# Kernel optimization log

Measured on AMD Instinct MI355X. Metric: run time of the kernel, lower is better.

Reference implementation:

```python
import jax, jax.numpy as jnp
import numpy as np

B, N, C, H = 4, 2048, 768, 12
D = C // H  # head_dim = 64

def setup_inputs() -> dict:
    key = jax.random.key(0)
    ks = jax.random.split(key, 6)
    s = 0.02
    return {
        "img_tokens": jax.random.normal(ks[0], (B, N, C), jnp.float32),
        "ln_gamma": jnp.ones((C,), jnp.float32),
        "ln_beta": jnp.zeros((C,), jnp.float32),
        "w_qkv": jax.random.normal(ks[1], (C, 3 * C), jnp.float32) * s,
        "w_out": jax.random.normal(ks[2], (C, C), jnp.float32) * s,
        "b_out": jnp.zeros((C,), jnp.float32),
    }

def reference(img_tokens, ln_gamma, ln_beta, w_qkv, w_out, b_out):
    x = img_tokens
    # LayerNorm over channel dim
    mu = jnp.mean(x, axis=-1, keepdims=True)
    var = jnp.var(x, axis=-1, keepdims=True)
    xn = (x - mu) * jax.lax.rsqrt(var + 1e-5) * ln_gamma + ln_beta
    qkv = xn @ w_qkv                      # [B, N, 3C]
    q, k, v = jnp.split(qkv, 3, axis=-1)
    def heads(t):                          # [B, N, C] -> [B, H, N, D]
        return t.reshape(B, N, H, D).transpose(0, 2, 1, 3)
    q, k, v = heads(q), heads(k), heads(v)
    scale = 1.0 / np.sqrt(D).astype(np.float32)
    scores = jnp.einsum('bhnd,bhmd->bhnm', q, k) * scale  # [B, H, N, N]
    attn = jax.nn.softmax(scores, axis=-1)
    out = jnp.einsum('bhnm,bhmd->bhnd', attn, v)          # [B, H, N, D]
    out = out.transpose(0, 2, 1, 3).reshape(B, N, C)
    out = out @ w_out + b_out
    return out + img_tokens
```

## Files before the change

kernel.cpp:

```cpp
#include <hip/hip_runtime.h>


typedef __bf16 bf16x8 __attribute__((ext_vector_type(8)));
typedef float  f32x4  __attribute__((ext_vector_type(4)));

#define MFMA16(a,b,c) __builtin_amdgcn_mfma_f32_16x16x32_bf16((a),(b),(c),0,0,0)

__device__ inline f32x4 zero4() { f32x4 z = {0.f,0.f,0.f,0.f}; return z; }

__device__ inline void gll16(const __bf16* g, __bf16* l) {
  __builtin_amdgcn_global_load_lds((const __attribute__((address_space(1))) unsigned int*)g,
                                   (__attribute__((address_space(3))) unsigned int*)l,
                                   16, 0, 0);
}

__device__ inline __bf16 bf16_trunc(float f) {
  const unsigned int u = __builtin_bit_cast(unsigned int, f);
  return __builtin_bit_cast(__bf16, (unsigned short)(u >> 16));
}

__global__ __launch_bounds__(256) void ln_kernel(const float* __restrict__ x,
                                                 const float* __restrict__ g,
                                                 const float* __restrict__ bt,
                                                 __bf16* __restrict__ xn) {
  const int row = blockIdx.x;
  const int tid = threadIdx.x;
  const float* xr = x + (size_t)row * 768;
  float v[3]; float s = 0.f, ss = 0.f;
  #pragma unroll
  for (int i = 0; i < 3; ++i) { float f = xr[tid + 256*i]; v[i] = f; s += f; ss += f*f; }
  #pragma unroll
  for (int m = 32; m >= 1; m >>= 1) { s += __shfl_xor(s, m, 64); ss += __shfl_xor(ss, m, 64); }
  __shared__ float red[8];
  const int wave = tid >> 6;
  if ((tid & 63) == 0) { red[wave] = s; red[4 + wave] = ss; }
  __syncthreads();
  s  = red[0] + red[1] + red[2] + red[3];
  ss = red[4] + red[5] + red[6] + red[7];
  const float mu  = s * (1.f/768.f);
  const float var = ss * (1.f/768.f) - mu*mu;
  const float inv = rsqrtf(var + 1e-5f);
  __bf16* xo = xn + (size_t)row * 768;
  #pragma unroll
  for (int i = 0; i < 3; ++i) {
    const int c0 = tid + 256*i;
    xo[c0] = (__bf16)((v[i] - mu) * inv * g[c0] + bt[c0]);
  }
}

__global__ __launch_bounds__(256) void transpose_kernel(const float* __restrict__ in,
                                                        __bf16* __restrict__ out,
                                                        int R, int C) {
  __shared__ float t[32][33];
  const int tx = threadIdx.x & 31, ty = threadIdx.x >> 5;
  const int c0 = blockIdx.x * 32, r0 = blockIdx.y * 32;
  #pragma unroll
  for (int p = 0; p < 4; ++p) t[ty + 8*p][tx] = in[(size_t)(r0 + ty + 8*p) * C + c0 + tx];
  __syncthreads();
  #pragma unroll
  for (int p = 0; p < 4; ++p) out[(size_t)(c0 + ty + 8*p) * R + r0 + tx] = (__bf16)t[tx][ty + 8*p];
}

template<int KDIM>
__device__ inline void gemm_mainloop(const __bf16* __restrict__ A, const __bf16* __restrict__ BT,
                                     int bm, int bn, int wave, int lane,
                                     f32x4 acc[4][4], __bf16* Asm, __bf16* Bsm) {
  const int wm = wave >> 1, wn = wave & 1;
  const int lr = lane & 15, lk = lane >> 4;
  for (int k0 = 0; k0 < KDIM; k0 += 32) {
    #pragma unroll
    for (int s2 = 0; s2 < 2; ++s2) {
      const int blk = wave * 2 + s2;
      gll16(A  + (size_t)(bm + blk*16 + lr) * KDIM + k0 + lk*8, Asm + blk*512);
      gll16(BT + (size_t)(bn + blk*16 + lr) * KDIM + k0 + lk*8, Bsm + blk*512);
    }
    __builtin_amdgcn_s_waitcnt(0);
    __syncthreads();
    bf16x8 a[4], b[4];
    #pragma unroll
    for (int mt = 0; mt < 4; ++mt) a[mt] = *(const bf16x8*)(Asm + (wm*4+mt)*512 + lane*8);
    #pragma unroll
    for (int nt = 0; nt < 4; ++nt) b[nt] = *(const bf16x8*)(Bsm + (wn*4+nt)*512 + lane*8);
    #pragma unroll
    for (int mt = 0; mt < 4; ++mt)
      #pragma unroll
      for (int nt = 0; nt < 4; ++nt)
        acc[mt][nt] = MFMA16(a[mt], b[nt], acc[mt][nt]);
    __syncthreads();
  }
}

__global__ __launch_bounds__(256) void gemm_qkv_kernel(const __bf16* __restrict__ A,
                                                       const __bf16* __restrict__ BT,
                                                       __bf16* __restrict__ q,
                                                       __bf16* __restrict__ k,
                                                       __bf16* __restrict__ vt) {
  __shared__ __align__(16) __bf16 smem[128*66 + 256];
  __bf16* Asm = smem;
  __bf16* Bsm = smem + 4096;
  const int lane = threadIdx.x & 63, wave = threadIdx.x >> 6;
  const int bm = blockIdx.y * 128, bn = blockIdx.x * 128;
  f32x4 acc[4][4];
  #pragma unroll
  for (int i = 0; i < 4; ++i)
    #pragma unroll
    for (int j = 0; j < 4; ++j) acc[i][j] = zero4();
  gemm_mainloop<768>(A, BT, bm, bn, wave, lane, acc, Asm, Bsm);
  const int wm = wave >> 1, wn = wave & 1;
  const int quad = lane >> 4, c = lane & 15;
  if (bn < 1536) {
    const float qscale = 0.125f * 1.44269504088896f;
    #pragma unroll
    for (int mt = 0; mt < 4; ++mt)
      #pragma unroll
      for (int nt = 0; nt < 4; ++nt) {
        const int col = bn + wn*64 + nt*16 + c;
        const int which = col >> 9 >= 1 && col >= 768 ? 1 : 0;
        const int within = col - which*768;
        const int h = within >> 6, d = within & 63;
        #pragma unroll
        for (int r = 0; r < 4; ++r) {
          const int row = bm + wm*64 + mt*16 + quad*4 + r;
          const int b = row >> 11, n = row & 2047;
          const float vv = acc[mt][nt][r];
          const size_t idx = ((size_t)(b*12 + h) * 2048 + n) * 64 + d;
          if (which == 0) q[idx] = (__bf16)(vv * qscale);
          else            k[idx] = (__bf16)vv;
        }
      }
  } else {
    #pragma unroll
    for (int mt = 0; mt < 4; ++mt)
      #pragma unroll
      for (int nt = 0; nt < 4; ++nt) {
        const int lcol = wn*64 + nt*16 + c;
        #pragma unroll
        for (int r = 0; r < 4; ++r) {
          const int lrow = wm*64 + mt*16 + quad*4 + r;
          smem[lrow*66 + lcol] = (__bf16)acc[mt][nt][r];
        }
      }
    __syncthreads();
    const int b = bm >> 11, n0 = bm & 2047;
    const int vo = bn - 1536;
    const int n = threadIdx.x & 127;
    const int csel = threadIdx.x >> 7;
    #pragma unroll
    for (int pass = 0; pass < 64; ++pass) {
      const int lc = pass*2 + csel;
      const int gcol = vo + lc;
      const int h = gcol >> 6, d = gcol & 63;
      vt[((size_t)(b*12 + h)*64 + d)*2048 + n0 + n] = smem[n*66 + lc];
    }
  }
}

__global__ __launch_bounds__(256) void gemm_out_kernel(const __bf16* __restrict__ A,
                                                       const __bf16* __restrict__ BT,
                                                       const float* __restrict__ bias,
                                                       const float* __restrict__ resid,
                                                       float* __restrict__ out) {
  __shared__ __align__(16) __bf16 Asm[8*512];
  __shared__ __align__(16) __bf16 Bsm[8*512];
  const int lane = threadIdx.x & 63, wave = threadIdx.x >> 6;
  const int bm = blockIdx.y * 128, bn = blockIdx.x * 128;
  f32x4 acc[4][4];
  #pragma unroll
  for (int i = 0; i < 4; ++i)
    #pragma unroll
    for (int j = 0; j < 4; ++j) acc[i][j] = zero4();
  gemm_mainloop<768>(A, BT, bm, bn, wave, lane, acc, Asm, Bsm);
  const int wm = wave >> 1, wn = wave & 1;
  const int quad = lane >> 4, c = lane & 15;
  #pragma unroll
  for (int mt = 0; mt < 4; ++mt)
    #pragma unroll
    for (int nt = 0; nt < 4; ++nt) {
      const int col = bn + wn*64 + nt*16 + c;
      #pragma unroll
      for (int r = 0; r < 4; ++r) {
        const int row = bm + wm*64 + mt*16 + quad*4 + r;
        out[(size_t)row*768 + col] = acc[mt][nt][r] + bias[col] + resid[(size_t)row*768 + col];
      }
    }
}

__global__ __launch_bounds__(256) void attn_kernel(const __bf16* __restrict__ q,
                                                   const __bf16* __restrict__ k,
                                                   const __bf16* __restrict__ vt,
                                                   __bf16* __restrict__ o) {
  const int bh = blockIdx.x >> 4;
  const int qt = blockIdx.x & 15;
  const int lane = threadIdx.x & 63, wave = threadIdx.x >> 6;
  const int c = lane & 15, quad = lane >> 4;
  const int lr = lane & 15, lk = lane >> 4;
  const int q0 = qt*128 + wave*32;

  const __bf16* qb = q  + ((size_t)bh*2048 + q0) * 64;
  const __bf16* kb = k  + (size_t)bh * 2048 * 64;
  const __bf16* vb = vt + (size_t)bh * 64 * 2048;

  __shared__ __align__(16) __bf16 Ksm[2][4096];
  __shared__ __align__(16) __bf16 Vsm[2][4096];
  __shared__ __align__(16) __bf16 plds[4][2048];
  __bf16* myp = plds[wave];

  bf16x8 aq[2][2];
  #pragma unroll
  for (int rg = 0; rg < 2; ++rg) {
    aq[rg][0] = *(const bf16x8*)(qb + (size_t)(rg*16 + c)*64 + quad*8);
    aq[rg][1] = *(const bf16x8*)(qb + (size_t)(rg*16 + c)*64 + 32 + quad*8);
  }

  float cl[2][4];
  f32x4 od[2][4];
  #pragma unroll
  for (int rg = 0; rg < 2; ++rg)
    #pragma unroll
    for (int r = 0; r < 4; ++r) { cl[rg][r] = 0.f; od[rg][r] = zero4(); }

  auto stage = [&](int it) {
    const int kt = it * 64;
    __bf16* Ks = Ksm[it & 1];
    __bf16* Vs = Vsm[it & 1];
    gll16(kb + (size_t)(kt + wave*16 + lr) * 64 + lk*8,        Ks + (wave*2+0)*512);
    gll16(kb + (size_t)(kt + wave*16 + lr) * 64 + 32 + lk*8,   Ks + (wave*2+1)*512);
    gll16(vb + (size_t)(wave*16 + lr) * 2048 + kt + lk*8,      Vs + (wave*2+0)*512);
    gll16(vb + (size_t)(wave*16 + lr) * 2048 + kt + 32 + lk*8, Vs + (wave*2+1)*512);
  };

  stage(0);
  stage(1);

  for (int it = 0; it < 32; ++it) {
    const __bf16* Ks = Ksm[it & 1];
    const __bf16* Vs = Vsm[it & 1];
    if (it < 31) asm volatile("s_waitcnt vmcnt(4)" ::: "memory");
    else         asm volatile("s_waitcnt vmcnt(0)" ::: "memory");
    asm volatile("s_barrier" ::: "memory");
    f32x4 s0[4], s1[4];
    #pragma unroll
    for (int t = 0; t < 4; ++t) {
      const bf16x8 b0 = *(const bf16x8*)(Ks + (t*2+0)*512 + lane*8);
      const bf16x8 b1 = *(const bf16x8*)(Ks + (t*2+1)*512 + lane*8);
      f32x4 z0 = zero4(), z1 = zero4();
      z0 = MFMA16(aq[0][0], b0, z0); z0 = MFMA16(aq[0][1], b1, z0);
      z1 = MFMA16(aq[1][0], b0, z1); z1 = MFMA16(aq[1][1], b1, z1);
      s0[t] = z0; s1[t] = z1;
    }
    #pragma unroll
    for (int t = 0; t < 4; ++t) {
      const int kk = t*16 + c;
      const int base = (kk >> 5)*512 + ((kk >> 3) & 3)*128 + (kk & 7);
      #pragma unroll
      for (int r = 0; r < 4; ++r) {
        const float p0 = __builtin_amdgcn_exp2f(s0[t][r]);
        const float p1 = __builtin_amdgcn_exp2f(s1[t][r]);
        cl[0][r] += p0; cl[1][r] += p1;
        myp[base + (quad*4 + r)*8]        = bf16_trunc(p0);
        myp[1024 + base + (quad*4 + r)*8] = bf16_trunc(p1);
      }
    }
    asm volatile("s_waitcnt lgkmcnt(0)" ::: "memory");
    const bf16x8 ap00 = *(const bf16x8*)(myp + lane*8);
    const bf16x8 ap01 = *(const bf16x8*)(myp + 512 + lane*8);
    const bf16x8 ap10 = *(const bf16x8*)(myp + 1024 + lane*8);
    const bf16x8 ap11 = *(const bf16x8*)(myp + 1536 + lane*8);
    #pragma unroll
    for (int dt = 0; dt < 4; ++dt) {
      const bf16x8 bv0 = *(const bf16x8*)(Vs + (dt*2+0)*512 + lane*8);
      const bf16x8 bv1 = *(const bf16x8*)(Vs + (dt*2+1)*512 + lane*8);
      od[0][dt] = MFMA16(ap00, bv0, od[0][dt]);
      od[0][dt] = MFMA16(ap01, bv1, od[0][dt]);
      od[1][dt] = MFMA16(ap10, bv0, od[1][dt]);
      od[1][dt] = MFMA16(ap11, bv1, od[1][dt]);
    }
    asm volatile("s_barrier" ::: "memory");
    if (it + 2 < 32) stage(it + 2);
  }
  const int b = bh / 12, h = bh % 12;
  #pragma unroll
  for (int rg = 0; rg < 2; ++rg) {
    float rl[4];
    #pragma unroll
    for (int r = 0; r < 4; ++r) {
      float v0 = cl[rg][r];
      v0 += __shfl_xor(v0, 1); v0 += __shfl_xor(v0, 2);
      v0 += __shfl_xor(v0, 4); v0 += __shfl_xor(v0, 8);
      rl[r] = 1.f / v0;
    }
    #pragma unroll
    for (int dt = 0; dt < 4; ++dt)
      #pragma unroll
      for (int r = 0; r < 4; ++r) {
        const int n = q0 + rg*16 + quad*4 + r;
        const int col = h*64 + dt*16 + c;
        o[((size_t)b*2048 + n)*768 + col] = (__bf16)(od[rg][dt][r] * rl[r]);
      }
  }
}

extern "C" void kernel_launch(void* const* d_in, const int* in_sizes, int n_in,
                              void* d_out, int out_size, void* d_ws, size_t ws_size,
                              hipStream_t stream) {
  const float* img   = (const float*)d_in[0];
  const float* gamma = (const float*)d_in[1];
  const float* beta  = (const float*)d_in[2];
  const float* wqkv  = (const float*)d_in[3];
  const float* wout  = (const float*)d_in[4];
  const float* bout  = (const float*)d_in[5];
  float* out = (float*)d_out;

  __bf16* ws = (__bf16*)d_ws;
  size_t off = 0;
  __bf16* xn    = ws + off; off += (size_t)8192*768;
  __bf16* wqkvT = ws + off; off += (size_t)2304*768;
  __bf16* woutT = ws + off; off += (size_t)768*768;
  __bf16* qs    = ws + off; off += (size_t)48*2048*64;
  __bf16* ks    = ws + off; off += (size_t)48*2048*64;
  __bf16* vts   = ws + off; off += (size_t)48*64*2048;
  __bf16* os    = ws + off; off += (size_t)8192*768;

  ln_kernel<<<8192, 256, 0, stream>>>(img, gamma, beta, xn);
  transpose_kernel<<<dim3(72, 24), 256, 0, stream>>>(wqkv, wqkvT, 768, 2304);
  transpose_kernel<<<dim3(24, 24), 256, 0, stream>>>(wout, woutT, 768, 768);
  gemm_qkv_kernel<<<dim3(18, 64), 256, 0, stream>>>(xn, wqkvT, qs, ks, vts);
  attn_kernel<<<768, 256, 0, stream>>>(qs, ks, vts, os);
  gemm_out_kernel<<<dim3(6, 64), 256, 0, stream>>>(os, woutT, bout, img, out);
}
```

Baseline: 271.6 us.

## Deepen GEMM K-tile, remap attention blocks per XCD, swizzle P staging

The QKV and output GEMM mainloops now stage a 64-wide K slice per barrier instead of 32. That halves the number of sync points and doubles the LDS tiles. The attention kernel remaps block indices so each XCD handles a contiguous group of heads, which is meant to improve L2 reuse of K/V. It also splits the per-iteration work into two 32-key chunks, with an XOR-swizzled, half-sized P buffer to cut LDS bank conflicts and register pressure. A barrier is added before the V-tile epilogue reuses shared memory, since the staging buffers now overlap it.

```diff
diff --git a/kernel.cpp b/kernel.cpp
--- a/kernel.cpp
+++ b/kernel.cpp
@@ -67,25 +67,29 @@
                                      f32x4 acc[4][4], __bf16* Asm, __bf16* Bsm) {
   const int wm = wave >> 1, wn = wave & 1;
   const int lr = lane & 15, lk = lane >> 4;
-  for (int k0 = 0; k0 < KDIM; k0 += 32) {
-    #pragma unroll
-    for (int s2 = 0; s2 < 2; ++s2) {
-      const int blk = wave * 2 + s2;
-      gll16(A  + (size_t)(bm + blk*16 + lr) * KDIM + k0 + lk*8, Asm + blk*512);
-      gll16(BT + (size_t)(bn + blk*16 + lr) * KDIM + k0 + lk*8, Bsm + blk*512);
+  for (int k0 = 0; k0 < KDIM; k0 += 64) {
+    #pragma unroll
+    for (int s2 = 0; s2 < 4; ++s2) {
+      const int st = wave * 4 + s2;
+      const int rb = st >> 1, kh = st & 1;
+      gll16(A  + (size_t)(bm + rb*16 + lr) * KDIM + k0 + kh*32 + lk*8, Asm + st*512);
+      gll16(BT + (size_t)(bn + rb*16 + lr) * KDIM + k0 + kh*32 + lk*8, Bsm + st*512);
     }
     __builtin_amdgcn_s_waitcnt(0);
     __syncthreads();
-    bf16x8 a[4], b[4];
-    #pragma unroll
-    for (int mt = 0; mt < 4; ++mt) a[mt] = *(const bf16x8*)(Asm + (wm*4+mt)*512 + lane*8);
-    #pragma unroll
-    for (int nt = 0; nt < 4; ++nt) b[nt] = *(const bf16x8*)(Bsm + (wn*4+nt)*512 + lane*8);
-    #pragma unroll
-    for (int mt = 0; mt < 4; ++mt)
-      #pragma unroll
-      for (int nt = 0; nt < 4; ++nt)
-        acc[mt][nt] = MFMA16(a[mt], b[nt], acc[mt][nt]);
+    #pragma unroll
+    for (int ks = 0; ks < 2; ++ks) {
+      bf16x8 a[4], b[4];
+      #pragma unroll
+      for (int mt = 0; mt < 4; ++mt) a[mt] = *(const bf16x8*)(Asm + ((wm*4+mt)*2+ks)*512 + lane*8);
+      #pragma unroll
+      for (int nt = 0; nt < 4; ++nt) b[nt] = *(const bf16x8*)(Bsm + ((wn*4+nt)*2+ks)*512 + lane*8);
+      #pragma unroll
+      for (int mt = 0; mt < 4; ++mt)
+        #pragma unroll
+        for (int nt = 0; nt < 4; ++nt)
+          acc[mt][nt] = MFMA16(a[mt], b[nt], acc[mt][nt]);
+    }
     __syncthreads();
   }
 }
@@ -95,9 +99,9 @@
                                                        __bf16* __restrict__ q,
                                                        __bf16* __restrict__ k,
                                                        __bf16* __restrict__ vt) {
-  __shared__ __align__(16) __bf16 smem[128*66 + 256];
+  __shared__ __align__(16) __bf16 smem[2*8192];
   __bf16* Asm = smem;
-  __bf16* Bsm = smem + 4096;
+  __bf16* Bsm = smem + 8192;
   const int lane = threadIdx.x & 63, wave = threadIdx.x >> 6;
   const int bm = blockIdx.y * 128, bn = blockIdx.x * 128;
   f32x4 acc[4][4];
@@ -115,7 +119,7 @@
       #pragma unroll
       for (int nt = 0; nt < 4; ++nt) {
         const int col = bn + wn*64 + nt*16 + c;
-        const int which = col >> 9 >= 1 && col >= 768 ? 1 : 0;
+        const int which = col >= 768 ? 1 : 0;
         const int within = col - which*768;
         const int h = within >> 6, d = within & 63;
         #pragma unroll
@@ -129,6 +133,7 @@
         }
       }
   } else {
+    __syncthreads();
     #pragma unroll
     for (int mt = 0; mt < 4; ++mt)
       #pragma unroll
@@ -160,8 +165,8 @@
                                                        const float* __restrict__ bias,
                                                        const float* __restrict__ resid,
                                                        float* __restrict__ out) {
-  __shared__ __align__(16) __bf16 Asm[8*512];
-  __shared__ __align__(16) __bf16 Bsm[8*512];
+  __shared__ __align__(16) __bf16 Asm[16*512];
+  __shared__ __align__(16) __bf16 Bsm[16*512];
   const int lane = threadIdx.x & 63, wave = threadIdx.x >> 6;
   const int bm = blockIdx.y * 128, bn = blockIdx.x * 128;
   f32x4 acc[4][4];
@@ -189,8 +194,9 @@
                                                    const __bf16* __restrict__ k,
                                                    const __bf16* __restrict__ vt,
                                                    __bf16* __restrict__ o) {
-  const int bh = blockIdx.x >> 4;
-  const int qt = blockIdx.x & 15;
+  const int xcd = blockIdx.x & 7, i = blockIdx.x >> 3;
+  const int bh = xcd * 6 + (i >> 4);
+  const int qt = i & 15;
   const int lane = threadIdx.x & 63, wave = threadIdx.x >> 6;
   const int c = lane & 15, quad = lane >> 4;
   const int lr = lane & 15, lk = lane >> 4;
@@ -202,7 +208,7 @@
 
   __shared__ __align__(16) __bf16 Ksm[2][4096];
   __shared__ __align__(16) __bf16 Vsm[2][4096];
-  __shared__ __align__(16) __bf16 plds[4][2048];
+  __shared__ __align__(16) __bf16 plds[4][1024];
   __bf16* myp = plds[wave];
 
   bf16x8 aq[2][2];
@@ -232,48 +238,53 @@
   stage(0);
   stage(1);
 
+  const int sl = lane ^ ((lane >> 3) & 7);
+
   for (int it = 0; it < 32; ++it) {
     const __bf16* Ks = Ksm[it & 1];
     const __bf16* Vs = Vsm[it & 1];
     if (it < 31) asm volatile("s_waitcnt vmcnt(4)" ::: "memory");
     else         asm volatile("s_waitcnt vmcnt(0)" ::: "memory");
     asm volatile("s_barrier" ::: "memory");
-    f32x4 s0[4], s1[4];
-    #pragma unroll
-    for (int t = 0; t < 4; ++t) {
-      const bf16x8 b0 = *(const bf16x8*)(Ks + (t*2+0)*512 + lane*8);
-      const bf16x8 b1 = *(const bf16x8*)(Ks + (t*2+1)*512 + lane*8);
-      f32x4 z0 = zero4(), z1 = zero4();
-      z0 = MFMA16(aq[0][0], b0, z0); z0 = MFMA16(aq[0][1], b1, z0);
-      z1 = MFMA16(aq[1][0], b0, z1); z1 = MFMA16(aq[1][1], b1, z1);
-      s0[t] = z0; s1[t] = z1;
-    }
-    #pragma unroll
-    for (int t = 0; t < 4; ++t) {
-      const int kk = t*16 + c;
-      const int base = (kk >> 5)*512 + ((kk >> 3) & 3)*128 + (kk & 7);
-      #pragma unroll
-      for (int r = 0; r < 4; ++r) {
-        const float p0 = __builtin_amdgcn_exp2f(s0[t][r]);
-        const float p1 = __builtin_amdgcn_exp2f(s1[t][r]);
-        cl[0][r] += p0; cl[1][r] += p1;
-        myp[base + (quad*4 + r)*8]        = bf16_trunc(p0);
-        myp[1024 + base + (quad*4 + r)*8] = bf16_trunc(p1);
-      }
-    }
-    asm volatile("s_waitcnt lgkmcnt(0)" ::: "memory");
-    const bf16x8 ap00 = *(const bf16x8*)(myp + lane*8);
-    const bf16x8 ap01 = *(const bf16x8*)(myp + 512 + lane*8);
-    const bf16x8 ap10 = *(const bf16x8*)(myp + 1024 + lane*8);
-    const bf16x8 ap11 = *(const bf16x8*)(myp + 1536 + lane*8);
-    #pragma unroll
-    for (int dt = 0; dt < 4; ++dt) {
-      const bf16x8 bv0 = *(const bf16x8*)(Vs + (dt*2+0)*512 + lane*8);
-      const bf16x8 bv1 = *(const bf16x8*)(Vs + (dt*2+1)*512 + lane*8);
-      od[0][dt] = MFMA16(ap00, bv0, od[0][dt]);
-      od[0][dt] = MFMA16(ap01, bv1, od[0][dt]);
-      od[1][dt] = MFMA16(ap10, bv0, od[1][dt]);
-      od[1][dt] = MFMA16(ap11, bv1, od[1][dt]);
+    #pragma unroll
+    for (int ch = 0; ch < 2; ++ch) {
+      f32x4 s0[2], s1[2];
+      #pragma unroll
+      for (int t2 = 0; t2 < 2; ++t2) {
+        const int t = ch*2 + t2;
+        const bf16x8 b0 = *(const bf16x8*)(Ks + (t*2+0)*512 + lane*8);
+        const bf16x8 b1 = *(const bf16x8*)(Ks + (t*2+1)*512 + lane*8);
+        f32x4 z0 = zero4(), z1 = zero4();
+        z0 = MFMA16(aq[0][0], b0, z0); z0 = MFMA16(aq[0][1], b1, z0);
+        z1 = MFMA16(aq[1][0], b0, z1); z1 = MFMA16(aq[1][1], b1, z1);
+        s0[t2] = z0; s1[t2] = z1;
+      }
+      #pragma unroll
+      for (int t2 = 0; t2 < 2; ++t2) {
+        const int kk = t2*16 + c;
+        const int k8 = kk >> 3, j = kk & 7;
+        #pragma unroll
+        for (int r = 0; r < 4; ++r) {
+          const int row = quad*4 + r;
+          const int b = k8*16 + row;
+          const int sb = b ^ ((b >> 3) & 7);
+          const float p0 = __builtin_amdgcn_exp2f(s0[t2][r]);
+          const float p1 = __builtin_amdgcn_exp2f(s1[t2][r]);
+          cl[0][r] += p0; cl[1][r] += p1;
+          myp[sb*8 + j]       = bf16_trunc(p0);
+          myp[512 + sb*8 + j] = bf16_trunc(p1);
+        }
+      }
+      asm volatile("s_waitcnt lgkmcnt(0)" ::: "memory");
+      const bf16x8 ap0 = *(const bf16x8*)(myp + sl*8);
+      const bf16x8 ap1 = *(const bf16x8*)(myp + 512 + sl*8);
+      asm volatile("" ::: "memory");
+      #pragma unroll
+      for (int dt = 0; dt < 4; ++dt) {
+        const bf16x8 bv = *(const bf16x8*)(Vs + (dt*2+ch)*512 + lane*8);
+        od[0][dt] = MFMA16(ap0, bv, od[0][dt]);
+        od[1][dt] = MFMA16(ap1, bv, od[1][dt]);
+      }
     }
     asm volatile("s_barrier" ::: "memory");
     if (it + 2 < 32) stage(it + 2);
```

Measured after the change: 269.4 us. No clear change (-0.8%).
